# Kernel tuning notes

Hardware: AMD Instinct MI355X
Metric: run time of the kernel (lower is better)

## Reference

```python
import jax, jax.numpy as jnp
import numpy as np

# CapsuleConv2d(128, 256, 3, in_length=16, out_length=16, stride=1, padding=1,
#               share_weight=True, routing_type='k_means' (dot), num_iterations=3, squash=True)
KH = KW = 3
SH = SW = 1
PH = PW = 1
DH = DW = 1
IN_LENGTH = 16
OUT_LENGTH = 16
NUM_ITERS = 3
EPS = 1e-12


def _extract_patches(x):
    # x: [B, C, H, W] -> [B, C, KH, KW, OH, OW] (torch.nn.functional.unfold layout)
    B, C, H, W = x.shape
    OH = (H + 2 * PH - DH * (KH - 1) - 1) // SH + 1
    OW = (W + 2 * PW - DW * (KW - 1) - 1) // SW + 1
    xp = jnp.pad(x, ((0, 0), (0, 0), (PH, PH), (PW, PW)))
    rows = []
    for i in range(KH):  # small fixed kernel loop
        cols = []
        for j in range(KW):
            cols.append(xp[:, :, i * DH: i * DH + (OH - 1) * SH + 1: SH,
                              j * DW: j * DW + (OW - 1) * SW + 1: SW])
        rows.append(jnp.stack(cols, axis=2))
    return jnp.stack(rows, axis=2)  # [B, C, KH, KW, OH, OW]


def _k_means_routing(u, num_iterations):
    # u: [B, OH, OW, N_in, O, L]; routing over N_in (axis -3), dot similarity
    v = u.mean(axis=-3, keepdims=True)  # [B, OH, OW, 1, O, L]
    for _ in range(num_iterations):
        vn = v / jnp.maximum(jnp.linalg.norm(v, axis=-1, keepdims=True), EPS)
        logits = jnp.sum(u * vn, axis=-1, keepdims=True)      # [B,OH,OW,N_in,O,1]
        probs = jax.nn.softmax(logits, axis=-3)
        v = jnp.sum(probs * u, axis=-3, keepdims=True)
    return jnp.squeeze(v, axis=-3)  # [B, OH, OW, O, L]


def _squash(s):
    norm = jnp.linalg.norm(s, axis=-1, keepdims=True)
    return s * (norm / (1.0 + norm * norm))  # = ||s||^2/(1+||s||^2) * s/||s||


def setup_inputs() -> dict:
    key = jax.random.key(0)
    k1, k2 = jax.random.split(key)
    x = jax.random.normal(k1, (2, 128, 32, 32), dtype=jnp.float32)
    # weight: [O=out_channels//out_length, L=out_length, M=in_length, KH, KW]
    fan = IN_LENGTH * KH * KW + OUT_LENGTH * KH * KW
    bound = float(np.sqrt(6.0 / fan))  # xavier_uniform-ish scale
    weight = jax.random.uniform(k2, (16, 16, 16, 3, 3), dtype=jnp.float32,
                                minval=-bound, maxval=bound)
    return {"x": x, "weight": weight}


def reference(x, weight):
    B = x.shape[0]
    O, L, M = weight.shape[0], weight.shape[1], weight.shape[2]
    patches = _extract_patches(x)                      # [B, C, KH, KW, OH, OW]
    OH, OW = patches.shape[-2], patches.shape[-1]
    G = x.shape[1] // M
    patches = patches.reshape(B, G, M, KH, KW, OH, OW)
    # priors[b,h,w,g,i,j,o,l] = sum_m patch[b,g,m,i,j,h,w] * weight[o,l,m,i,j]
    priors = jnp.einsum('bgmijhw,olmij->bhwgijol', patches, weight)
    priors = priors.reshape(B, OH, OW, G * KH * KW, O, L)
    v = _k_means_routing(priors, NUM_ITERS)            # [B, OH, OW, O, L]
    v = _squash(v)
    out = v.reshape(B, OH, OW, O * L).transpose(0, 3, 1, 2)  # [B, C_out, OH, OW]
    return out
```

## Files before the change

kernel.cpp:

```cpp
#include <hip/hip_runtime.h>


typedef float v2f __attribute__((ext_vector_type(2)));
typedef int   i4  __attribute__((ext_vector_type(4)));
typedef short bh8 __attribute__((ext_vector_type(8)));
typedef float f16v __attribute__((ext_vector_type(16)));

#define STR 34
#define WBF_ELEMS 73728

#define DPP_ADD(a, ctrl)                                                     \
  a += __int_as_float(__builtin_amdgcn_update_dpp(                           \
          0, __float_as_int(a), ctrl, 0xF, 0xF, true))

__device__ __forceinline__ float dpp_add16(float x) {
    float s = x;
    DPP_ADD(s, 0x128); DPP_ADD(s, 0x124); DPP_ADD(s, 0x122); DPP_ADD(s, 0x121);
    return s;
}

__device__ __forceinline__ float swz16_add(float x) {
    int y = __builtin_amdgcn_ds_swizzle(__float_as_int(x), 0x401F);
    return x + __int_as_float(y);
}

__device__ __forceinline__ float frcp(float x) {
    return __builtin_amdgcn_rcpf(x);
}

__device__ __forceinline__ v2f pkfma(v2f a, v2f b, v2f c) {
    return __builtin_elementwise_fma(a, b, c);
}

__global__ __launch_bounds__(256)
void prep2_kernel(const float* __restrict__ x, const float* __restrict__ W,
                  i4* __restrict__ xP, unsigned short* __restrict__ Wbf) {
    const int blk = blockIdx.x;
    const int tid = threadIdx.x;
    if (blk < 64) {
        __shared__ float xs[128 * 33];
        const int b = blk >> 5, h = blk & 31;
        const float* xb = x + b * (128 * 32 * 32) + h * 32;
        #pragma unroll
        for (int k = 0; k < 16; ++k) {
            int idx = k * 256 + tid;
            int c = idx >> 5, w = idx & 31;
            xs[c * 33 + w] = xb[c * 1024 + w];
        }
        __syncthreads();
        i4* xo = xP + (b * 32 + h) * 1024;
        #pragma unroll
        for (int it = 0; it < 4; ++it) {
            int slot = it * 256 + tid;
            int s  = slot & 1;
            int hf = (slot >> 1) & 1;
            int gl = (slot >> 2) & 7;
            int w  = slot >> 5;
            int c0 = gl * 16 + hf * 8;
            float f0 = xs[(c0 + 0) * 33 + w], f1 = xs[(c0 + 1) * 33 + w];
            float f2 = xs[(c0 + 2) * 33 + w], f3 = xs[(c0 + 3) * 33 + w];
            float f4 = xs[(c0 + 4) * 33 + w], f5 = xs[(c0 + 5) * 33 + w];
            float f6 = xs[(c0 + 6) * 33 + w], f7 = xs[(c0 + 7) * 33 + w];
            unsigned b0 = __float_as_uint(f0), b1 = __float_as_uint(f1);
            unsigned b2 = __float_as_uint(f2), b3 = __float_as_uint(f3);
            unsigned b4 = __float_as_uint(f4), b5 = __float_as_uint(f5);
            unsigned b6 = __float_as_uint(f6), b7 = __float_as_uint(f7);
            i4 pk;
            if (s == 0) {
                pk.x = (int)((b0 >> 16) | (b1 & 0xFFFF0000u));
                pk.y = (int)((b2 >> 16) | (b3 & 0xFFFF0000u));
                pk.z = (int)((b4 >> 16) | (b5 & 0xFFFF0000u));
                pk.w = (int)((b6 >> 16) | (b7 & 0xFFFF0000u));
            } else {
                unsigned l0 = __float_as_uint(f0 - __uint_as_float(b0 & 0xFFFF0000u));
                unsigned l1 = __float_as_uint(f1 - __uint_as_float(b1 & 0xFFFF0000u));
                unsigned l2 = __float_as_uint(f2 - __uint_as_float(b2 & 0xFFFF0000u));
                unsigned l3 = __float_as_uint(f3 - __uint_as_float(b3 & 0xFFFF0000u));
                unsigned l4 = __float_as_uint(f4 - __uint_as_float(b4 & 0xFFFF0000u));
                unsigned l5 = __float_as_uint(f5 - __uint_as_float(b5 & 0xFFFF0000u));
                unsigned l6 = __float_as_uint(f6 - __uint_as_float(b6 & 0xFFFF0000u));
                unsigned l7 = __float_as_uint(f7 - __uint_as_float(b7 & 0xFFFF0000u));
                pk.x = (int)((l0 >> 16) | (l1 & 0xFFFF0000u));
                pk.y = (int)((l2 >> 16) | (l3 & 0xFFFF0000u));
                pk.z = (int)((l4 >> 16) | (l5 & 0xFFFF0000u));
                pk.w = (int)((l6 >> 16) | (l7 & 0xFFFF0000u));
            }
            xo[slot] = pk;
        }
    } else {
        int idx = (blk - 64) * 256 + tid;
        int j  = idx & 7;
        int L  = (idx >> 3) & 63;
        int s  = (idx >> 9) & 1;
        int tt = (idx >> 10) & 7;
        int ij = idx >> 13;
        int k  = (L >> 5) * 8 + j;
        int t  = tt * 32 + (L & 31);
        float wv = W[(t * 16 + k) * 9 + ij];
        unsigned bits = __float_as_uint(wv);
        unsigned hib  = bits & 0xFFFF0000u;
        unsigned short val;
        if (s == 0) val = (unsigned short)(hib >> 16);
        else {
            float lo = wv - __uint_as_float(hib);
            val = (unsigned short)(__float_as_uint(lo) >> 16);
        }
        Wbf[idx] = val;
    }
}

#define ALOADIJ(AH, AL, OK, IJ) {                                            \
    const int di = (IJ) / 3, dj = (IJ) % 3;                                  \
    const int hh = h + di - 1;                                               \
    const bool hok = (unsigned)hh < 32u;                                     \
    const int hhc = hok ? hh : 0;                                            \
    const int ww = w0 + pl + dj - 1;                                         \
    OK = hok && ((unsigned)ww < 32u);                                        \
    const int wwc = OK ? ww : 0;                                             \
    const int slot = (((bb * 32 + hhc) * 32 + wwc) * 8 + gl) * 2 + half;     \
    AH = xpi4[slot * 2]; AL = xpi4[slot * 2 + 1]; }

#define BLOADIJ(BH, BL, IJ) {                                                \
    BH = bfr[((IJ) * 8 + tt) * 128 + lane];                                  \
    BL = bfr[((IJ) * 8 + tt) * 128 + 64 + lane]; }

#define CWR(REG, IJ)                                                         \
    uLds[wroff + STR * ((((REG) >> 2) * 72) + (((REG) & 3) * 9) + (IJ))] =   \
        acc[(REG)];

#define PROCIJ(AH, AL, OK, BH, BL, IJ) {                                     \
    const i4 z_ = {0, 0, 0, 0};                                              \
    i4 ah_ = OK ? AH : z_;                                                   \
    i4 al_ = OK ? AL : z_;                                                   \
    bh8 aHi = __builtin_bit_cast(bh8, ah_);                                  \
    bh8 aLo = __builtin_bit_cast(bh8, al_);                                  \
    bh8 bHi = __builtin_bit_cast(bh8, BH);                                   \
    bh8 bLo = __builtin_bit_cast(bh8, BL);                                   \
    f16v acc = {0.f,0.f,0.f,0.f,0.f,0.f,0.f,0.f,                             \
                0.f,0.f,0.f,0.f,0.f,0.f,0.f,0.f};                            \
    acc = __builtin_amdgcn_mfma_f32_32x32x16_bf16(aHi, bLo, acc, 0, 0, 0);   \
    acc = __builtin_amdgcn_mfma_f32_32x32x16_bf16(aLo, bHi, acc, 0, 0, 0);   \
    acc = __builtin_amdgcn_mfma_f32_32x32x16_bf16(aHi, bHi, acc, 0, 0, 0);   \
    CWR(0, IJ)  CWR(1, IJ)  CWR(2, IJ)  CWR(3, IJ)                           \
    CWR(4, IJ)  CWR(5, IJ)  CWR(6, IJ)  CWR(7, IJ)                           \
    CWR(8, IJ)  CWR(9, IJ)  CWR(10, IJ) CWR(11, IJ)                          \
    CWR(12, IJ) CWR(13, IJ) CWR(14, IJ) CWR(15, IJ) }

#define LROW(K)                                                              \
  { const v2f* r2_ = (const v2f*)(rb + (K) * 16 * STR);                      \
    U##K##0 = r2_[0]; U##K##1 = r2_[1]; U##K##2 = r2_[2]; U##K##3 = r2_[3]; }

#define DOTR(K)                                                              \
  ({ v2f d_ = U##K##0 * V0;                                                  \
     d_ = pkfma(U##K##1, V1, d_); d_ = pkfma(U##K##2, V2, d_);               \
     d_ = pkfma(U##K##3, V3, d_); swz16_add(d_.x + d_.y); })

#define MEANJ(J)                                                             \
  { v2f s_ = (U0##J + U1##J) + (U2##J + U3##J) + U4##J;                      \
    V##J.x = dpp_add16(s_.x) * (1.0f / 72.0f);                               \
    V##J.y = dpp_add16(s_.y) * (1.0f / 72.0f); }

#define UPDJ(J)                                                              \
  { v2f pv_ = e0v * U0##J;                                                   \
    pv_ = pkfma(e1v, U1##J, pv_); pv_ = pkfma(e2v, U2##J, pv_);              \
    pv_ = pkfma(e3v, U3##J, pv_); pv_ = pkfma(e4v, U4##J, pv_);              \
    V##J.x = dpp_add16(pv_.x) * rs;                                          \
    V##J.y = dpp_add16(pv_.y) * rs; }

__global__ __launch_bounds__(256, 4)
void capsule_v13(const i4* __restrict__ xpi4, const i4* __restrict__ bfr,
                 float* __restrict__ out) {
    __shared__ float uLds[4 * 72 * STR];
    const int blk = blockIdx.x;
    const int tt  = blk & 7;
    const int q   = blk >> 3;
    const int bb  = q >> 8;
    const int r   = q & 255;
    const int h   = r >> 3;
    const int w0  = (r & 7) << 2;
    const int tid = threadIdx.x;

    {
        const int lane = tid & 63;
        const int wv   = tid >> 6;
        const int pl   = (lane & 31) >> 3;
        const int gl   = lane & 7;
        const int half = lane >> 5;
        const int tl   = lane & 31;
        const int wroff = tl + STR * 9 * 4 * half;

        if (wv == 0) {
            i4 a0h, a0l, a1h, a1l, a2h, a2l;
            i4 b0h, b0l, b1h, b1l, b2h, b2l;
            bool ok0, ok1, ok2;
            ALOADIJ(a0h, a0l, ok0, 0) BLOADIJ(b0h, b0l, 0)
            ALOADIJ(a1h, a1l, ok1, 4) BLOADIJ(b1h, b1l, 4)
            PROCIJ(a0h, a0l, ok0, b0h, b0l, 0)
            ALOADIJ(a2h, a2l, ok2, 8) BLOADIJ(b2h, b2l, 8)
            PROCIJ(a1h, a1l, ok1, b1h, b1l, 4)
            PROCIJ(a2h, a2l, ok2, b2h, b2l, 8)
        } else if (wv == 1) {
            i4 a0h, a0l, a1h, a1l, b0h, b0l, b1h, b1l;
            bool ok0, ok1;
            ALOADIJ(a0h, a0l, ok0, 1) BLOADIJ(b0h, b0l, 1)
            ALOADIJ(a1h, a1l, ok1, 5) BLOADIJ(b1h, b1l, 5)
            PROCIJ(a0h, a0l, ok0, b0h, b0l, 1)
            PROCIJ(a1h, a1l, ok1, b1h, b1l, 5)
        } else if (wv == 2) {
            i4 a0h, a0l, a1h, a1l, b0h, b0l, b1h, b1l;
            bool ok0, ok1;
            ALOADIJ(a0h, a0l, ok0, 2) BLOADIJ(b0h, b0l, 2)
            ALOADIJ(a1h, a1l, ok1, 6) BLOADIJ(b1h, b1l, 6)
            PROCIJ(a0h, a0l, ok0, b0h, b0l, 2)
            PROCIJ(a1h, a1l, ok1, b1h, b1l, 6)
        } else {
            i4 a0h, a0l, a1h, a1l, b0h, b0l, b1h, b1l;
            bool ok0, ok1;
            ALOADIJ(a0h, a0l, ok0, 3) BLOADIJ(b0h, b0l, 3)
            ALOADIJ(a1h, a1l, ok1, 7) BLOADIJ(b1h, b1l, 7)
            PROCIJ(a0h, a0l, ok0, b0h, b0l, 3)
            PROCIJ(a1h, a1l, ok1, b1h, b1l, 7)
        }
    }
    __syncthreads();

    const int p  = tid >> 6;
    const int i6 = tid & 63;
    const int o2 = i6 >> 5;
    const int jh = (i6 >> 4) & 1;
    const int sc = i6 & 15;
    const bool has5 = (sc < 8);
    const float* rb = uLds + (p * 72 + sc) * STR + o2 * 16 + jh * 8;

    v2f U00, U01, U02, U03;
    v2f U10, U11, U12, U13;
    v2f U20, U21, U22, U23;
    v2f U30, U31, U32, U33;
    v2f U40, U41, U42, U43;
    U40 = U41 = U42 = U43 = (v2f){0.0f, 0.0f};
    LROW(0) LROW(1) LROW(2) LROW(3)
    if (has5) LROW(4)

    v2f V0, V1, V2, V3;
    MEANJ(0) MEANJ(1) MEANJ(2) MEANJ(3)

    #pragma unroll 1
    for (int it = 0; it < 3; ++it) {
        v2f ssv = V0 * V0;
        ssv = pkfma(V1, V1, ssv); ssv = pkfma(V2, V2, ssv);
        ssv = pkfma(V3, V3, ssv);
        float ss = swz16_add(ssv.x + ssv.y);
        float inv = frcp(fmaxf(sqrtf(ss), 1e-12f));

        float E0 = __expf(DOTR(0) * inv);
        float E1 = __expf(DOTR(1) * inv);
        float E2 = __expf(DOTR(2) * inv);
        float E3 = __expf(DOTR(3) * inv);
        float E4 = has5 ? __expf(DOTR(4) * inv) : 0.0f;
        float ssum = dpp_add16(((E0 + E1) + (E2 + E3)) + E4);
        float rs = frcp(ssum);

        v2f e0v = {E0, E0}, e1v = {E1, E1}, e2v = {E2, E2};
        v2f e3v = {E3, E3}, e4v = {E4, E4};
        UPDJ(0) UPDJ(1) UPDJ(2) UPDJ(3)
    }

    v2f ssv = V0 * V0;
    ssv = pkfma(V1, V1, ssv); ssv = pkfma(V2, V2, ssv);
    ssv = pkfma(V3, V3, ssv);
    float ss = swz16_add(ssv.x + ssv.y);
    float scale = sqrtf(ss) * frcp(1.0f + ss);

    v2f aa0 = (sc & 4) ? V2 : V0;
    v2f aa1 = (sc & 4) ? V3 : V1;
    v2f bb0 = (sc & 2) ? aa1 : aa0;
    float res = ((sc & 1) ? bb0.y : bb0.x) * scale;
    if (sc < 8) {
        int tg = tt * 32 + o2 * 16 + jh * 8 + sc;
        out[((bb * 256 + tg) * 32 + h) * 32 + w0 + p] = res;
    }
}

__global__ __launch_bounds__(256, 1)
void capsule_fb(const float* __restrict__ x, const float* __restrict__ Wraw,
                float* __restrict__ out) {
    __shared__ float patch[9 * 128];
    const int blk = blockIdx.x;
    const int b = blk >> 10, h = (blk >> 5) & 31, w = blk & 31;
    const int t = threadIdx.x;

    const float* xb = x + b * (128 * 32 * 32);
    for (int idx = t; idx < 1152; idx += 256) {
        int c = idx / 9, ij = idx - c * 9;
        int di = ij / 3, dj = ij - di * 3;
        int hh = h + di - 1, ww = w + dj - 1;
        float v = 0.0f;
        if ((unsigned)hh < 32u && (unsigned)ww < 32u)
            v = xb[(c * 32 + hh) * 32 + ww];
        patch[ij * 128 + c] = v;
    }
    __syncthreads();

    float u[72];
    #pragma unroll
    for (int ij = 0; ij < 9; ++ij) {
        float wr[16];
        #pragma unroll
        for (int m = 0; m < 16; ++m) wr[m] = Wraw[(t * 16 + m) * 9 + ij];
        #pragma unroll
        for (int g = 0; g < 8; ++g) {
            float acc = 0.0f;
            #pragma unroll
            for (int m = 0; m < 16; ++m)
                acc = fmaf(patch[ij * 128 + g * 16 + m], wr[m], acc);
            u[g * 9 + ij] = acc;
        }
    }

    float v = 0.0f;
    #pragma unroll
    for (int n = 0; n < 72; ++n) v += u[n];
    v *= (1.0f / 72.0f);
    #pragma unroll 1
    for (int it = 0; it < 3; ++it) {
        float sg = dpp_add16(v * v);
        float vn = v * frcp(fmaxf(sqrtf(sg), 1e-12f));
        float ssum = 0.0f, vacc = 0.0f;
        #pragma unroll
        for (int n = 0; n < 72; ++n) {
            float pp = dpp_add16(u[n] * vn);
            float e = __expf(pp);
            ssum += e;
            vacc = fmaf(e, u[n], vacc);
        }
        v = vacc * frcp(ssum);
    }
    float sg = dpp_add16(v * v);
    float res = v * sqrtf(sg) * frcp(1.0f + sg);
    out[((b * 256 + t) * 32 + h) * 32 + w] = res;
}

extern "C" void kernel_launch(void* const* d_in, const int* in_sizes, int n_in,
                              void* d_out, int out_size, void* d_ws, size_t ws_size,
                              hipStream_t stream) {
    const float* x = (const float*)d_in[0];
    const float* W = (const float*)d_in[1];
    float* out = (float*)d_out;
    i4* xP = (i4*)d_ws;
    unsigned short* Wbf = (unsigned short*)((char*)d_ws + 1048576);

    const size_t need = 1048576 + (size_t)WBF_ELEMS * 2;
    if (ws_size >= need) {
        prep2_kernel<<<352, 256, 0, stream>>>(x, W, xP, Wbf);
        capsule_v13<<<4096, 256, 0, stream>>>(xP, (const i4*)Wbf, out);
    } else {
        capsule_fb<<<2048, 256, 0, stream>>>(x, W, out);
    }
}
```

Baseline: 79.60 us.

## Split routing across 512 threads with 32 lanes per capsule row set

Launches the fused capsule kernel with 512 threads per block. The k-means routing now spreads the 72 input capsules over 32 lanes, each holding 3 rows instead of 5, so per-thread register use and serial FMA chains shrink. Reductions over input capsules become a 32-lane DPP-plus-swizzle reduction. The dot products over capsule length combine halves with a cross-32 shuffle. The prior-computing MFMA stage still uses only the first four waves, so the extra waves sit idle there, and the shuffle-based reduction may cost more than the old swizzle.

```diff
diff --git a/kernel.cpp b/kernel.cpp
--- a/kernel.cpp
+++ b/kernel.cpp
@@ -22,6 +22,14 @@
 __device__ __forceinline__ float swz16_add(float x) {
     int y = __builtin_amdgcn_ds_swizzle(__float_as_int(x), 0x401F);
     return x + __int_as_float(y);
+}
+
+__device__ __forceinline__ float red32(float x) {
+    return swz16_add(dpp_add16(x));
+}
+
+__device__ __forceinline__ float xor32_add(float x) {
+    return x + __shfl_xor(x, 32, 64);
 }
 
 __device__ __forceinline__ float frcp(float x) {
@@ -146,29 +154,28 @@
     CWR(8, IJ)  CWR(9, IJ)  CWR(10, IJ) CWR(11, IJ)                          \
     CWR(12, IJ) CWR(13, IJ) CWR(14, IJ) CWR(15, IJ) }
 
-#define LROW(K)                                                              \
-  { const v2f* r2_ = (const v2f*)(rb + (K) * 16 * STR);                      \
-    U##K##0 = r2_[0]; U##K##1 = r2_[1]; U##K##2 = r2_[2]; U##K##3 = r2_[3]; }
-
-#define DOTR(K)                                                              \
-  ({ v2f d_ = U##K##0 * V0;                                                  \
-     d_ = pkfma(U##K##1, V1, d_); d_ = pkfma(U##K##2, V2, d_);               \
-     d_ = pkfma(U##K##3, V3, d_); swz16_add(d_.x + d_.y); })
+#define LROWV(U0_, U1_, U2_, U3_, OFF)                                       \
+  { const v2f* r2_ = (const v2f*)(rb + (OFF) * STR);                         \
+    U0_ = r2_[0]; U1_ = r2_[1]; U2_ = r2_[2]; U3_ = r2_[3]; }
+
+#define DOTV(UK0, UK1, UK2, UK3)                                             \
+  ({ v2f d_ = UK0 * V0;                                                      \
+     d_ = pkfma(UK1, V1, d_); d_ = pkfma(UK2, V2, d_);                       \
+     d_ = pkfma(UK3, V3, d_); xor32_add(d_.x + d_.y); })
 
 #define MEANJ(J)                                                             \
-  { v2f s_ = (U0##J + U1##J) + (U2##J + U3##J) + U4##J;                      \
-    V##J.x = dpp_add16(s_.x) * (1.0f / 72.0f);                               \
-    V##J.y = dpp_add16(s_.y) * (1.0f / 72.0f); }
+  { v2f s_ = (U0##J + U1##J) + U2##J;                                        \
+    V##J.x = red32(s_.x) * (1.0f / 72.0f);                                   \
+    V##J.y = red32(s_.y) * (1.0f / 72.0f); }
 
 #define UPDJ(J)                                                              \
   { v2f pv_ = e0v * U0##J;                                                   \
     pv_ = pkfma(e1v, U1##J, pv_); pv_ = pkfma(e2v, U2##J, pv_);              \
-    pv_ = pkfma(e3v, U3##J, pv_); pv_ = pkfma(e4v, U4##J, pv_);              \
-    V##J.x = dpp_add16(pv_.x) * rs;                                          \
-    V##J.y = dpp_add16(pv_.y) * rs; }
-
-__global__ __launch_bounds__(256, 4)
-void capsule_v13(const i4* __restrict__ xpi4, const i4* __restrict__ bfr,
+    V##J.x = red32(pv_.x) * rs;                                              \
+    V##J.y = red32(pv_.y) * rs; }
+
+__global__ __launch_bounds__(512, 8)
+void capsule_v14(const i4* __restrict__ xpi4, const i4* __restrict__ bfr,
                  float* __restrict__ out) {
     __shared__ float uLds[4 * 72 * STR];
     const int blk = blockIdx.x;
@@ -189,57 +196,57 @@
         const int tl   = lane & 31;
         const int wroff = tl + STR * 9 * 4 * half;
 
-        if (wv == 0) {
-            i4 a0h, a0l, a1h, a1l, a2h, a2l;
-            i4 b0h, b0l, b1h, b1l, b2h, b2l;
-            bool ok0, ok1, ok2;
-            ALOADIJ(a0h, a0l, ok0, 0) BLOADIJ(b0h, b0l, 0)
-            ALOADIJ(a1h, a1l, ok1, 4) BLOADIJ(b1h, b1l, 4)
-            PROCIJ(a0h, a0l, ok0, b0h, b0l, 0)
-            ALOADIJ(a2h, a2l, ok2, 8) BLOADIJ(b2h, b2l, 8)
-            PROCIJ(a1h, a1l, ok1, b1h, b1l, 4)
-            PROCIJ(a2h, a2l, ok2, b2h, b2l, 8)
-        } else if (wv == 1) {
-            i4 a0h, a0l, a1h, a1l, b0h, b0l, b1h, b1l;
-            bool ok0, ok1;
-            ALOADIJ(a0h, a0l, ok0, 1) BLOADIJ(b0h, b0l, 1)
-            ALOADIJ(a1h, a1l, ok1, 5) BLOADIJ(b1h, b1l, 5)
-            PROCIJ(a0h, a0l, ok0, b0h, b0l, 1)
-            PROCIJ(a1h, a1l, ok1, b1h, b1l, 5)
-        } else if (wv == 2) {
-            i4 a0h, a0l, a1h, a1l, b0h, b0l, b1h, b1l;
-            bool ok0, ok1;
-            ALOADIJ(a0h, a0l, ok0, 2) BLOADIJ(b0h, b0l, 2)
-            ALOADIJ(a1h, a1l, ok1, 6) BLOADIJ(b1h, b1l, 6)
-            PROCIJ(a0h, a0l, ok0, b0h, b0l, 2)
-            PROCIJ(a1h, a1l, ok1, b1h, b1l, 6)
-        } else {
-            i4 a0h, a0l, a1h, a1l, b0h, b0l, b1h, b1l;
-            bool ok0, ok1;
-            ALOADIJ(a0h, a0l, ok0, 3) BLOADIJ(b0h, b0l, 3)
-            ALOADIJ(a1h, a1l, ok1, 7) BLOADIJ(b1h, b1l, 7)
-            PROCIJ(a0h, a0l, ok0, b0h, b0l, 3)
-            PROCIJ(a1h, a1l, ok1, b1h, b1l, 7)
+        if (wv < 4) {
+            if (wv == 0) {
+                i4 a0h, a0l, a1h, a1l, a2h, a2l;
+                i4 b0h, b0l, b1h, b1l, b2h, b2l;
+                bool ok0, ok1, ok2;
+                ALOADIJ(a0h, a0l, ok0, 0) BLOADIJ(b0h, b0l, 0)
+                ALOADIJ(a1h, a1l, ok1, 4) BLOADIJ(b1h, b1l, 4)
+                PROCIJ(a0h, a0l, ok0, b0h, b0l, 0)
+                ALOADIJ(a2h, a2l, ok2, 8) BLOADIJ(b2h, b2l, 8)
+                PROCIJ(a1h, a1l, ok1, b1h, b1l, 4)
+                PROCIJ(a2h, a2l, ok2, b2h, b2l, 8)
+            } else if (wv == 1) {
+                i4 a0h, a0l, a1h, a1l, b0h, b0l, b1h, b1l;
+                bool ok0, ok1;
+                ALOADIJ(a0h, a0l, ok0, 1) BLOADIJ(b0h, b0l, 1)
+                ALOADIJ(a1h, a1l, ok1, 5) BLOADIJ(b1h, b1l, 5)
+                PROCIJ(a0h, a0l, ok0, b0h, b0l, 1)
+                PROCIJ(a1h, a1l, ok1, b1h, b1l, 5)
+            } else if (wv == 2) {
+                i4 a0h, a0l, a1h, a1l, b0h, b0l, b1h, b1l;
+                bool ok0, ok1;
+                ALOADIJ(a0h, a0l, ok0, 2) BLOADIJ(b0h, b0l, 2)
+                ALOADIJ(a1h, a1l, ok1, 6) BLOADIJ(b1h, b1l, 6)
+                PROCIJ(a0h, a0l, ok0, b0h, b0l, 2)
+                PROCIJ(a1h, a1l, ok1, b1h, b1l, 6)
+            } else {
+                i4 a0h, a0l, a1h, a1l, b0h, b0l, b1h, b1l;
+                bool ok0, ok1;
+                ALOADIJ(a0h, a0l, ok0, 3) BLOADIJ(b0h, b0l, 3)
+                ALOADIJ(a1h, a1l, ok1, 7) BLOADIJ(b1h, b1l, 7)
+                PROCIJ(a0h, a0l, ok0, b0h, b0l, 3)
+                PROCIJ(a1h, a1l, ok1, b1h, b1l, 7)
+            }
         }
     }
     __syncthreads();
 
-    const int p  = tid >> 6;
-    const int i6 = tid & 63;
-    const int o2 = i6 >> 5;
-    const int jh = (i6 >> 4) & 1;
-    const int sc = i6 & 15;
-    const bool has5 = (sc < 8);
+    const int p  = tid >> 7;
+    const int o2 = (tid >> 6) & 1;
+    const int jh = (tid >> 5) & 1;
+    const int sc = tid & 31;
+    const bool has3 = (sc < 8);
     const float* rb = uLds + (p * 72 + sc) * STR + o2 * 16 + jh * 8;
 
     v2f U00, U01, U02, U03;
     v2f U10, U11, U12, U13;
     v2f U20, U21, U22, U23;
-    v2f U30, U31, U32, U33;
-    v2f U40, U41, U42, U43;
-    U40 = U41 = U42 = U43 = (v2f){0.0f, 0.0f};
-    LROW(0) LROW(1) LROW(2) LROW(3)
-    if (has5) LROW(4)
+    U20 = U21 = U22 = U23 = (v2f){0.0f, 0.0f};
+    LROWV(U00, U01, U02, U03, 0)
+    LROWV(U10, U11, U12, U13, 32)
+    if (has3) LROWV(U20, U21, U22, U23, 64)
 
     v2f V0, V1, V2, V3;
     MEANJ(0) MEANJ(1) MEANJ(2) MEANJ(3)
@@ -249,26 +256,23 @@
         v2f ssv = V0 * V0;
         ssv = pkfma(V1, V1, ssv); ssv = pkfma(V2, V2, ssv);
         ssv = pkfma(V3, V3, ssv);
-        float ss = swz16_add(ssv.x + ssv.y);
+        float ss = xor32_add(ssv.x + ssv.y);
         float inv = frcp(fmaxf(sqrtf(ss), 1e-12f));
 
-        float E0 = __expf(DOTR(0) * inv);
-        float E1 = __expf(DOTR(1) * inv);
-        float E2 = __expf(DOTR(2) * inv);
-        float E3 = __expf(DOTR(3) * inv);
-        float E4 = has5 ? __expf(DOTR(4) * inv) : 0.0f;
-        float ssum = dpp_add16(((E0 + E1) + (E2 + E3)) + E4);
+        float E0 = __expf(DOTV(U00, U01, U02, U03) * inv);
+        float E1 = __expf(DOTV(U10, U11, U12, U13) * inv);
+        float E2 = has3 ? __expf(DOTV(U20, U21, U22, U23) * inv) : 0.0f;
+        float ssum = red32((E0 + E1) + E2);
         float rs = frcp(ssum);
 
         v2f e0v = {E0, E0}, e1v = {E1, E1}, e2v = {E2, E2};
-        v2f e3v = {E3, E3}, e4v = {E4, E4};
         UPDJ(0) UPDJ(1) UPDJ(2) UPDJ(3)
     }
 
     v2f ssv = V0 * V0;
     ssv = pkfma(V1, V1, ssv); ssv = pkfma(V2, V2, ssv);
     ssv = pkfma(V3, V3, ssv);
-    float ss = swz16_add(ssv.x + ssv.y);
+    float ss = xor32_add(ssv.x + ssv.y);
     float scale = sqrtf(ss) * frcp(1.0f + ss);
 
     v2f aa0 = (sc & 4) ? V2 : V0;
@@ -352,7 +356,7 @@
     const size_t need = 1048576 + (size_t)WBF_ELEMS * 2;
     if (ws_size >= need) {
         prep2_kernel<<<352, 256, 0, stream>>>(x, W, xP, Wbf);
-        capsule_v13<<<4096, 256, 0, stream>>>(xP, (const i4*)Wbf, out);
+        capsule_v14<<<4096, 512, 0, stream>>>(xP, (const i4*)Wbf, out);
     } else {
         capsule_fb<<<2048, 256, 0, stream>>>(x, W, out);
     }
```

Result: slower. 91.16 us (+14.5%).
